# Kernel tuning notes

Measured on AMD Instinct MI355X. Metric: run time of the kernel, lower is better.

The kernel has to match this reference:

```python
import jax, jax.numpy as jnp
import numpy as np

EPS = 1e-8  # matches F.cosine_similarity default eps
SIM_TARGET = 1  # int(self.sim_matrix), a scalar constant


def setup_inputs() -> dict:
    key = jax.random.key(0)
    k1, k2 = jax.random.split(key)
    input1 = jax.random.normal(k1, (4096, 1024), dtype=jnp.float32)  # [U, P]
    input2 = jax.random.normal(k2, (4096, 1024), dtype=jnp.float32)  # [V, P]
    return {"input1": input1, "input2": input2}


def reference(input1, input2):
    # Row-normalize with eps clamp (same as F.cosine_similarity per pair)
    n1 = input1 / jnp.maximum(jnp.linalg.norm(input1, axis=1, keepdims=True), EPS)
    n2 = input2 / jnp.maximum(jnp.linalg.norm(input2, axis=1, keepdims=True), EPS)
    cos = jnp.einsum('up,vp->uv', n1, n2)  # [U, V] pairwise cosine similarity
    return jnp.sum((SIM_TARGET - cos) ** 2)
```

## Files before the change

kernel.cpp:

```cpp
#include <hip/hip_runtime.h>
#include <hip/hip_bf16.h>
#include <stdint.h>

#define U_ROWS 4096
#define P_DIM  1024
#define TB     256
#define BK     64
#define NKT    (P_DIM / BK)

typedef int i32x4  __attribute__((ext_vector_type(4)));
typedef int i32x16 __attribute__((ext_vector_type(16)));

__global__ __launch_bounds__(256) void norm_i8_kernel(
    const float* __restrict__ in1, const float* __restrict__ in2,
    int8_t* __restrict__ out, float* __restrict__ loss_out) {
    const int w = threadIdx.x >> 6, lane = threadIdx.x & 63;
    const int row = blockIdx.x * 4 + w;
    const float* src = (row < U_ROWS) ? (in1 + (size_t)row * P_DIM)
                                      : (in2 + (size_t)(row - U_ROWS) * P_DIM);
    const float4* src4 = (const float4*)src;
    float4 v[4];
    float ss = 0.0f;
    #pragma unroll
    for (int j = 0; j < 4; ++j) {
        v[j] = src4[j * 64 + lane];
        ss += v[j].x * v[j].x + v[j].y * v[j].y + v[j].z * v[j].z + v[j].w * v[j].w;
    }
    #pragma unroll
    for (int off = 32; off > 0; off >>= 1) ss += __shfl_xor(ss, off, 64);
    const float inv = 512.0f / fmaxf(sqrtf(ss), 1e-8f);

    const int key = (row >> 1) & 3;
    int8_t* orow = out + (size_t)row * P_DIM;
    #pragma unroll
    for (int j = 0; j < 4; ++j) {
        int q0 = max(-127, min(127, (int)rintf(v[j].x * inv)));
        int q1 = max(-127, min(127, (int)rintf(v[j].y * inv)));
        int q2 = max(-127, min(127, (int)rintf(v[j].z * inv)));
        int q3 = max(-127, min(127, (int)rintf(v[j].w * inv)));
        const int d = (q0 & 255) | ((q1 & 255) << 8) | ((q2 & 255) << 16) | (q3 << 24);
        const int p0   = j * 256 + lane * 4;
        const int w0   = p0 >> 6;
        const int g    = (p0 >> 4) & 3;
        const int slot = g ^ key;
        *(int*)(orow + w0 * 64 + slot * 16 + (p0 & 15)) = d;
    }
    if (blockIdx.x == 0 && threadIdx.x == 0) *loss_out = 0.0f;
}

__global__ __launch_bounds__(512) void cosloss_gemm_i8(
    const int8_t* __restrict__ n1, const int8_t* __restrict__ n2,
    float* __restrict__ loss_out) {
    __shared__ __align__(16) uint8_t As[3][TB * BK];
    __shared__ __align__(16) uint8_t Bs[3][TB * BK];

    const int tid  = threadIdx.x;
    const int w    = tid >> 6;
    const int lane = tid & 63;

    const int id  = blockIdx.x;
    const int xcd = id & 7;
    const int t   = id >> 3;
    const int cb  = xcd * 2 + (t & 1);
    const int rb  = t >> 1;

    const uint8_t* gA = (const uint8_t*)n1 + (size_t)rb * TB * P_DIM;
    const uint8_t* gB = (const uint8_t*)n2 + (size_t)cb * TB * P_DIM;

    const int srow = lane >> 2;
    const int scol = (lane & 3) * 16;
    const int c0   = w * 4;

    auto stage = [&](int kt, int b) {
        #pragma unroll
        for (int cc = 0; cc < 4; ++cc) {
            const int c = c0 + cc;
            const uint8_t* gsrc = (c < 16)
                ? gA + (size_t)(c * 16 + srow) * P_DIM + kt * BK + scol
                : gB + (size_t)((c - 16) * 16 + srow) * P_DIM + kt * BK + scol;
            uint8_t* sdst = (c < 16) ? As[b] + c * 1024 : Bs[b] + (c - 16) * 1024;
            __builtin_amdgcn_global_load_lds(
                (const __attribute__((address_space(1))) void*)gsrc,
                (__attribute__((address_space(3))) void*)sdst, 16, 0, 0);
        }
    };

    i32x16 acc[4][2];
    #pragma unroll
    for (int mi = 0; mi < 4; ++mi)
        #pragma unroll
        for (int ni = 0; ni < 2; ++ni)
            acc[mi][ni] = (i32x16){0,0,0,0,0,0,0,0,0,0,0,0,0,0,0,0};

    const int wr = (w & 1) * 128;
    const int wc = (w >> 1) * 64;
    const int lm = lane & 31;
    const int lh = lane >> 5;

    int aoff[4][2], boff[2][2];
    #pragma unroll
    for (int i = 0; i < 4; ++i) {
        const int m = wr + i * 32 + lm;
        #pragma unroll
        for (int s = 0; s < 2; ++s)
            aoff[i][s] = m * BK + (((2 * s + lh) ^ ((m >> 1) & 3)) * 16);
    }
    #pragma unroll
    for (int ni = 0; ni < 2; ++ni) {
        const int n = wc + ni * 32 + lm;
        #pragma unroll
        for (int s = 0; s < 2; ++s)
            boff[ni][s] = n * BK + (((2 * s + lh) ^ ((n >> 1) & 3)) * 16);
    }

    stage(0, 0);
    stage(1, 1);

    for (int kt = 0; kt < NKT; ++kt) {
        if (kt < NKT - 1) {
            asm volatile("s_waitcnt vmcnt(4)" ::: "memory");
        } else {
            asm volatile("s_waitcnt vmcnt(0)" ::: "memory");
        }
        __builtin_amdgcn_s_barrier();
        __builtin_amdgcn_sched_barrier(0);

        if (kt + 2 < NKT) stage(kt + 2, (kt + 2) % 3);

        const uint8_t* Ab = As[kt % 3];
        const uint8_t* Bb = Bs[kt % 3];
        #pragma unroll
        for (int s = 0; s < 2; ++s) {
            i32x4 af[4], bf[2];
            #pragma unroll
            for (int i = 0; i < 4; ++i)
                af[i] = *(const i32x4*)(Ab + aoff[i][s]);
            #pragma unroll
            for (int ni = 0; ni < 2; ++ni)
                bf[ni] = *(const i32x4*)(Bb + boff[ni][s]);
            #pragma unroll
            for (int mi = 0; mi < 4; ++mi)
                #pragma unroll
                for (int ni = 0; ni < 2; ++ni)
                    acc[mi][ni] = __builtin_amdgcn_mfma_i32_32x32x32_i8(
                        af[mi], bf[ni], acc[mi][ni], 0, 0, 0);
        }
    }

    float local = 0.0f;
    #pragma unroll
    for (int mi = 0; mi < 4; ++mi)
        #pragma unroll
        for (int ni = 0; ni < 2; ++ni)
            #pragma unroll
            for (int r = 0; r < 16; ++r) {
                const float dd = 1.0f - (float)acc[mi][ni][r] * (1.0f / 262144.0f);
                local += dd * dd;
            }
    #pragma unroll
    for (int off = 32; off > 0; off >>= 1) local += __shfl_down(local, off, 64);

    __syncthreads();
    float* redf = (float*)As;
    if (lane == 0) redf[w] = local;
    __syncthreads();
    if (tid == 0) {
        float tsum = 0.0f;
        #pragma unroll
        for (int i = 0; i < 8; ++i) tsum += redf[i];
        atomicAdd(loss_out, tsum);
    }
}

extern "C" void kernel_launch(void* const* d_in, const int* in_sizes, int n_in,
                              void* d_out, int out_size, void* d_ws, size_t ws_size,
                              hipStream_t stream) {
    const float* in1 = (const float*)d_in[0];
    const float* in2 = (const float*)d_in[1];
    float* out = (float*)d_out;
    int8_t* nrm = (int8_t*)d_ws;

    norm_i8_kernel<<<(U_ROWS * 2) / 4, 256, 0, stream>>>(in1, in2, nrm, out);

    cosloss_gemm_i8<<<(U_ROWS / TB) * (U_ROWS / TB), 512, 0, stream>>>(
        nrm, nrm + (size_t)U_ROWS * P_DIM, out);
}
```

Baseline: 94.07 us.

## Interleave LDS reads, prefetch and MFMA in ping-pong clusters with setprio

Splits each k-tile's compute into four small clusters. Each cluster issues LDS fragment loads (and half of the next-tile global-to-LDS prefetch), then hits a workgroup barrier and runs four MFMAs at raised wave priority. The aim is to keep waves staggered so memory issue overlaps with matrix work, in the style of a ping-pong schedule. The cost is many extra s_barriers per iteration, fewer registers held live for fragments, and B fragments being reused across clusters.

```diff
diff --git a/kernel.cpp b/kernel.cpp
--- a/kernel.cpp
+++ b/kernel.cpp
@@ -71,9 +71,9 @@
     const int scol = (lane & 3) * 16;
     const int c0   = w * 4;
 
-    auto stage = [&](int kt, int b) {
-        #pragma unroll
-        for (int cc = 0; cc < 4; ++cc) {
+    auto stage2 = [&](int kt, int b, int half) {
+        #pragma unroll
+        for (int cc = 2 * half; cc < 2 * half + 2; ++cc) {
             const int c = c0 + cc;
             const uint8_t* gsrc = (c < 16)
                 ? gA + (size_t)(c * 16 + srow) * P_DIM + kt * BK + scol
@@ -113,8 +113,8 @@
             boff[ni][s] = n * BK + (((2 * s + lh) ^ ((n >> 1) & 3)) * 16);
     }
 
-    stage(0, 0);
-    stage(1, 1);
+    stage2(0, 0, 0); stage2(0, 0, 1);
+    stage2(1, 1, 0); stage2(1, 1, 1);
 
     for (int kt = 0; kt < NKT; ++kt) {
         if (kt < NKT - 1) {
@@ -125,26 +125,77 @@
         __builtin_amdgcn_s_barrier();
         __builtin_amdgcn_sched_barrier(0);
 
-        if (kt + 2 < NKT) stage(kt + 2, (kt + 2) % 3);
-
         const uint8_t* Ab = As[kt % 3];
         const uint8_t* Bb = Bs[kt % 3];
-        #pragma unroll
-        for (int s = 0; s < 2; ++s) {
-            i32x4 af[4], bf[2];
-            #pragma unroll
-            for (int i = 0; i < 4; ++i)
-                af[i] = *(const i32x4*)(Ab + aoff[i][s]);
-            #pragma unroll
-            for (int ni = 0; ni < 2; ++ni)
-                bf[ni] = *(const i32x4*)(Bb + boff[ni][s]);
-            #pragma unroll
-            for (int mi = 0; mi < 4; ++mi)
-                #pragma unroll
-                for (int ni = 0; ni < 2; ++ni)
-                    acc[mi][ni] = __builtin_amdgcn_mfma_i32_32x32x32_i8(
-                        af[mi], bf[ni], acc[mi][ni], 0, 0, 0);
-        }
+        const int    pb   = (kt + 2) % 3;
+        const bool   pf   = (kt + 2) < NKT;
+
+        i32x4 a0, a1, b0, b1;
+
+        a0 = *(const i32x4*)(Ab + aoff[0][0]);
+        a1 = *(const i32x4*)(Ab + aoff[1][0]);
+        b0 = *(const i32x4*)(Bb + boff[0][0]);
+        b1 = *(const i32x4*)(Bb + boff[1][0]);
+        if (pf) stage2(kt + 2, pb, 0);
+        __builtin_amdgcn_sched_barrier(0);
+        __builtin_amdgcn_s_barrier();
+        asm volatile("s_waitcnt lgkmcnt(0)" ::: "memory");
+        __builtin_amdgcn_sched_barrier(0);
+        __builtin_amdgcn_s_setprio(1);
+        acc[0][0] = __builtin_amdgcn_mfma_i32_32x32x32_i8(a0, b0, acc[0][0], 0, 0, 0);
+        acc[0][1] = __builtin_amdgcn_mfma_i32_32x32x32_i8(a0, b1, acc[0][1], 0, 0, 0);
+        acc[1][0] = __builtin_amdgcn_mfma_i32_32x32x32_i8(a1, b0, acc[1][0], 0, 0, 0);
+        acc[1][1] = __builtin_amdgcn_mfma_i32_32x32x32_i8(a1, b1, acc[1][1], 0, 0, 0);
+        __builtin_amdgcn_s_setprio(0);
+        __builtin_amdgcn_sched_barrier(0);
+        __builtin_amdgcn_s_barrier();
+
+        a0 = *(const i32x4*)(Ab + aoff[2][0]);
+        a1 = *(const i32x4*)(Ab + aoff[3][0]);
+        __builtin_amdgcn_sched_barrier(0);
+        __builtin_amdgcn_s_barrier();
+        asm volatile("s_waitcnt lgkmcnt(0)" ::: "memory");
+        __builtin_amdgcn_sched_barrier(0);
+        __builtin_amdgcn_s_setprio(1);
+        acc[2][0] = __builtin_amdgcn_mfma_i32_32x32x32_i8(a0, b0, acc[2][0], 0, 0, 0);
+        acc[2][1] = __builtin_amdgcn_mfma_i32_32x32x32_i8(a0, b1, acc[2][1], 0, 0, 0);
+        acc[3][0] = __builtin_amdgcn_mfma_i32_32x32x32_i8(a1, b0, acc[3][0], 0, 0, 0);
+        acc[3][1] = __builtin_amdgcn_mfma_i32_32x32x32_i8(a1, b1, acc[3][1], 0, 0, 0);
+        __builtin_amdgcn_s_setprio(0);
+        __builtin_amdgcn_sched_barrier(0);
+        __builtin_amdgcn_s_barrier();
+
+        a0 = *(const i32x4*)(Ab + aoff[0][1]);
+        a1 = *(const i32x4*)(Ab + aoff[1][1]);
+        b0 = *(const i32x4*)(Bb + boff[0][1]);
+        b1 = *(const i32x4*)(Bb + boff[1][1]);
+        if (pf) stage2(kt + 2, pb, 1);
+        __builtin_amdgcn_sched_barrier(0);
+        __builtin_amdgcn_s_barrier();
+        asm volatile("s_waitcnt lgkmcnt(0)" ::: "memory");
+        __builtin_amdgcn_sched_barrier(0);
+        __builtin_amdgcn_s_setprio(1);
+        acc[0][0] = __builtin_amdgcn_mfma_i32_32x32x32_i8(a0, b0, acc[0][0], 0, 0, 0);
+        acc[0][1] = __builtin_amdgcn_mfma_i32_32x32x32_i8(a0, b1, acc[0][1], 0, 0, 0);
+        acc[1][0] = __builtin_amdgcn_mfma_i32_32x32x32_i8(a1, b0, acc[1][0], 0, 0, 0);
+        acc[1][1] = __builtin_amdgcn_mfma_i32_32x32x32_i8(a1, b1, acc[1][1], 0, 0, 0);
+        __builtin_amdgcn_s_setprio(0);
+        __builtin_amdgcn_sched_barrier(0);
+        __builtin_amdgcn_s_barrier();
+
+        a0 = *(const i32x4*)(Ab + aoff[2][1]);
+        a1 = *(const i32x4*)(Ab + aoff[3][1]);
+        __builtin_amdgcn_sched_barrier(0);
+        __builtin_amdgcn_s_barrier();
+        asm volatile("s_waitcnt lgkmcnt(0)" ::: "memory");
+        __builtin_amdgcn_sched_barrier(0);
+        __builtin_amdgcn_s_setprio(1);
+        acc[2][0] = __builtin_amdgcn_mfma_i32_32x32x32_i8(a0, b0, acc[2][0], 0, 0, 0);
+        acc[2][1] = __builtin_amdgcn_mfma_i32_32x32x32_i8(a0, b1, acc[2][1], 0, 0, 0);
+        acc[3][0] = __builtin_amdgcn_mfma_i32_32x32x32_i8(a1, b0, acc[3][0], 0, 0, 0);
+        acc[3][1] = __builtin_amdgcn_mfma_i32_32x32x32_i8(a1, b1, acc[3][1], 0, 0, 0);
+        __builtin_amdgcn_s_setprio(0);
+        __builtin_amdgcn_sched_barrier(0);
     }
 
     float local = 0.0f;
```

Result: no change. 94.78 us (+0.8%).
